# Performance work log

Hardware: AMD Instinct MI355X
Metric: run time of the kernel (lower is better)

## Reference

```python
import jax, jax.numpy as jnp
import numpy as np

N = 8192
D = 256
H = 4
E = 262144

def setup_inputs() -> dict:
    key = jax.random.key(0)
    ks = jax.random.split(key, 12)
    s = 1.0 / np.sqrt(D)
    inp = {
        "x": jax.random.normal(ks[0], (N, D), dtype=jnp.float32),
        "edge_index": jax.random.randint(ks[1], (2, E), 0, N, dtype=jnp.int64),
        "W_local": jax.random.normal(ks[2], (D, D), dtype=jnp.float32) * s,
        "b_local": jnp.zeros((D,), dtype=jnp.float32),
        "W_in": jax.random.normal(ks[3], (3 * D, D), dtype=jnp.float32) * s,
        "b_in": jnp.zeros((3 * D,), dtype=jnp.float32),
        "W_out": jax.random.normal(ks[4], (D, D), dtype=jnp.float32) * s,
        "b_out": jnp.zeros((D,), dtype=jnp.float32),
        "W1": jax.random.normal(ks[5], (2 * D, D), dtype=jnp.float32) * s,
        "b1": jnp.zeros((2 * D,), dtype=jnp.float32),
        "W2": jax.random.normal(ks[6], (D, 2 * D), dtype=jnp.float32) * (1.0 / np.sqrt(2 * D)),
        "b2": jnp.zeros((D,), dtype=jnp.float32),
    }
    return inp


def reference(x, edge_index, W_local, b_local, W_in, b_in, W_out, b_out, W1, b1, W2, b2):
    n = x.shape[0]
    dh = D // H
    # Dense adjacency build (faithful to original): adj[src, dst] = 1.0
    adj = jnp.zeros((n, n), dtype=x.dtype).at[edge_index[0], edge_index[1]].set(1.0)
    deg = jnp.clip(adj.sum(axis=1, keepdims=True), 1.0)  # (n, 1)
    adj_norm = adj / deg
    # Local message passing + linear
    local_out = (adj_norm @ x) @ W_local.T + b_local
    x = x + local_out
    # Multi-head self-attention (torch MultiheadAttention, batch of 1)
    qkv = x @ W_in.T + b_in  # (n, 3D)
    q, k, v = jnp.split(qkv, 3, axis=-1)
    q = q.reshape(n, H, dh)
    k = k.reshape(n, H, dh)
    v = v.reshape(n, H, dh)
    scores = jnp.einsum("qhd,khd->hqk", q, k) / np.sqrt(dh)  # (H, n, n)
    probs = jax.nn.softmax(scores, axis=-1)
    attn = jnp.einsum("hqk,khd->qhd", probs, v).reshape(n, D)
    attn_out = attn @ W_out.T + b_out
    x = x + attn_out
    # FFN with exact GELU
    h = jax.nn.gelu(x @ W1.T + b1, approximate=False)
    x = x + (h @ W2.T + b2)
    return x
```

## Files before the change

### kernel.cpp

```cpp
#include <hip/hip_runtime.h>
#include <stdint.h>

#define N_NODES 8192
#define DIM 256
#define NHEADS 4
#define DHEAD 64
#define NEDGES 262144
#define NSPLIT 4
#define KSPLIT (N_NODES / NSPLIT)

using bf16x8 = __attribute__((ext_vector_type(8))) __bf16;
using f32x4  = __attribute__((ext_vector_type(4))) float;

__device__ __forceinline__ unsigned short f2b(float f) {
    unsigned int u = __float_as_uint(f);
    unsigned int r = (u + 0x7FFFu + ((u >> 16) & 1u)) >> 16;
    return (unsigned short)r;
}

__device__ __forceinline__ float b2f(unsigned short s) {
    return __uint_as_float((unsigned int)s << 16);
}

__device__ __forceinline__ bf16x8 ld8(const unsigned short* p) {
    return *reinterpret_cast<const bf16x8*>(p);
}

__device__ __forceinline__ f32x4 mf(bf16x8 a, bf16x8 b, f32x4 c) {
    return __builtin_amdgcn_mfma_f32_16x16x32_bf16(a, b, c, 0, 0, 0);
}

__device__ __forceinline__ float fexp2(float x) {
    float r;
    asm volatile("v_exp_f32 %0, %1" : "=v"(r) : "v"(x));
    return r;
}

__device__ __forceinline__ void gl16(const void* g, void* l) {
    __builtin_amdgcn_global_load_lds(
        (const __attribute__((address_space(1))) unsigned int*)g,
        (__attribute__((address_space(3))) unsigned int*)l, 16, 0, 0);
}

#define QSCALE 0.18033688f

__global__ void detect_kernel(const void* edges, int* flag) {
    if (threadIdx.x == 0) {
        const long long* p = (const long long*)edges;
        int ok = 1;
        for (int i = 0; i < 64; ++i) {
            long long v = p[i];
            if (v < 0 || v >= N_NODES) ok = 0;
        }
        *flag = ok;
    }
}

__global__ void clear_kernel(uint4* p, int n16) {
    int i = blockIdx.x * blockDim.x + threadIdx.x;
    if (i < n16) p[i] = make_uint4(0, 0, 0, 0);
}

__global__ void edge_kernel(const void* edges, const int* flag, unsigned* mask) {
    int i = blockIdx.x * blockDim.x + threadIdx.x;
    if (i >= NEDGES) return;
    int src, dst;
    if (*flag) {
        const long long* p = (const long long*)edges;
        src = (int)p[i];
        dst = (int)p[NEDGES + i];
    } else {
        const int* p = (const int*)edges;
        src = p[i];
        dst = p[NEDGES + i];
    }
    atomicOr(&mask[src * (N_NODES / 32) + (dst >> 5)], 1u << (dst & 31));
}

__global__ __launch_bounds__(256) void agg_kernel(const unsigned* mask, const float* x,
                                                  unsigned short* m_bf) {
    __shared__ int nbr[N_NODES];
    __shared__ int wsum[4];
    int row = blockIdx.x;
    int tid = threadIdx.x, wave = tid >> 6, lane = tid & 63;

    unsigned bits = mask[row * (N_NODES / 32) + tid];
    int cnt = __popc(bits);
    int scan = cnt;
#pragma unroll
    for (int d = 1; d < 64; d <<= 1) {
        int v = __shfl_up(scan, d);
        if (lane >= d) scan += v;
    }
    if (lane == 63) wsum[wave] = scan;
    __syncthreads();
    int base = 0;
    for (int w = 0; w < 4; ++w) {
        int t = wsum[w];
        if (w < wave) base += t;
    }
    int deg = wsum[0] + wsum[1] + wsum[2] + wsum[3];
    int offset = base + scan - cnt;
    int nb = tid * 32;
    unsigned b2 = bits;
    while (b2) {
        int b = __ffs(b2) - 1;
        b2 &= b2 - 1;
        nbr[offset++] = nb + b;
    }
    __syncthreads();

    float a0 = 0.f, a1 = 0.f, a2 = 0.f, a3 = 0.f;
    int j = 0;
    for (; j + 4 <= deg; j += 4) {
        int n0 = nbr[j], n1 = nbr[j + 1], n2 = nbr[j + 2], n3 = nbr[j + 3];
        a0 += x[(size_t)n0 * DIM + tid];
        a1 += x[(size_t)n1 * DIM + tid];
        a2 += x[(size_t)n2 * DIM + tid];
        a3 += x[(size_t)n3 * DIM + tid];
    }
    for (; j < deg; ++j) a0 += x[(size_t)nbr[j] * DIM + tid];
    float acc = (a0 + a1) + (a2 + a3);
    float s = 1.0f / (float)(deg > 0 ? deg : 1);
    m_bf[(size_t)row * DIM + tid] = f2b(acc * s);
}

__global__ void cvt_kernel(const float* src, unsigned short* dst, int n) {
    int i = blockIdx.x * blockDim.x + threadIdx.x;
    if (i < n) dst[i] = f2b(src[i]);
}

template <int K>
__global__ __launch_bounds__(256, 4) void gemm_kernel(const unsigned short* __restrict__ A,
                                                      const unsigned short* __restrict__ W,
                                                      const float* __restrict__ bias,
                                                      const float* __restrict__ res,
                                                      float* __restrict__ outF,
                                                      unsigned short* __restrict__ outB,
                                                      int Nout, int qcols, int gelu) {
    __shared__ __align__(16) char smem[32768];
    int tid = threadIdx.x, wave = tid >> 6, lane = tid & 63;
    int c16 = lane & 15, g = lane >> 4;
    int r0b = blockIdx.x * 64;
    int c0 = blockIdx.y * 64;
    int lo3 = lane >> 3;
    int sw = ((lane & 7) ^ lo3) * 8;

    const unsigned short* sA = A + (size_t)(r0b + wave * 8 + lo3) * K + sw;
    const unsigned short* sB = W + (size_t)(c0 + wave * 8 + lo3) * K + sw;
    int dA = wave * 1024;
    int dB = 8192 + wave * 1024;

    auto stage = [&](int kt, int bufsel) {
        char* b = smem + bufsel * 16384;
        const unsigned short* a1 = sA + kt * 64;
        const unsigned short* b1 = sB + kt * 64;
        gl16(a1, b + dA);
        gl16(a1 + (size_t)32 * K, b + dA + 4096);
        gl16(b1, b + dB);
        gl16(b1 + (size_t)32 * K, b + dB + 4096);
    };

    f32x4 acc[4] = {};
    int arow = (wave * 16 + c16) * 128;
    int slot0 = ((0 + g) ^ (c16 & 7)) * 16;
    int slot1 = ((4 + g) ^ (c16 & 7)) * 16;

    stage(0, 0);
    asm volatile("s_waitcnt vmcnt(0)" ::: "memory");
    __syncthreads();

    constexpr int NT = K / 64;
#pragma unroll
    for (int kt = 0; kt < NT; ++kt) {
        if (kt + 1 < NT) stage(kt + 1, (kt + 1) & 1);
        char* buf = smem + (kt & 1) * 16384;
        bf16x8 af0 = ld8((unsigned short*)(buf + arow + slot0));
        bf16x8 af1 = ld8((unsigned short*)(buf + arow + slot1));
#pragma unroll
        for (int ct = 0; ct < 4; ++ct) {
            int brow = (ct * 16 + c16) * 128;
            bf16x8 bf0 = ld8((unsigned short*)(buf + 8192 + brow + slot0));
            bf16x8 bf1 = ld8((unsigned short*)(buf + 8192 + brow + slot1));
            acc[ct] = mf(af0, bf0, acc[ct]);
            acc[ct] = mf(af1, bf1, acc[ct]);
        }
        asm volatile("s_waitcnt vmcnt(0)" ::: "memory");
        __syncthreads();
    }

    int r0 = r0b + wave * 16;
#pragma unroll
    for (int ct = 0; ct < 4; ++ct) {
        int col = c0 + ct * 16 + c16;
        float bi = bias[col];
#pragma unroll
        for (int r = 0; r < 4; ++r) {
            int row = r0 + g * 4 + r;
            float gg = acc[ct][r] + bi;
            if (gelu) gg = 0.5f * gg * (1.0f + erff(gg * 0.70710678118654752f));
            if (res) gg += res[(size_t)row * Nout + col];
            if (outF) outF[(size_t)row * Nout + col] = gg;
            if (outB) {
                float gb = (col < qcols) ? gg * QSCALE : gg;
                outB[(size_t)row * Nout + col] = f2b(gb);
            }
        }
    }
}

__global__ __launch_bounds__(256) void vt_kernel(const unsigned short* qkv,
                                                 unsigned short* Vt) {
    __shared__ unsigned short T[64][72];
    int h = blockIdx.y;
    int n0 = blockIdx.x * 64;
    int t = threadIdx.x;
    int r = t & 63, cb = (t >> 6) * 16;
    const unsigned short* src = qkv + (size_t)(n0 + r) * 768 + 512 + h * 64 + cb;
    *(uint4*)&T[r][cb] = *(const uint4*)src;
    *(uint4*)&T[r][cb + 8] = *(const uint4*)(src + 8);
    __syncthreads();
    int d = t >> 2, nb = (t & 3) * 16;
    unsigned short tmp[16];
#pragma unroll
    for (int j = 0; j < 16; ++j) tmp[j] = T[nb + j][d];
    unsigned short* dst = Vt + (size_t)(h * 64 + d) * 8192 + n0 + nb;
    *(uint4*)dst = *(uint4*)&tmp[0];
    *(uint4*)(dst + 8) = *(uint4*)&tmp[8];
}

__global__ __launch_bounds__(256, 4) void flash_kernel(const unsigned short* __restrict__ qkv,
                                                       const unsigned short* __restrict__ vt,
                                                       unsigned short* __restrict__ Opart,
                                                       float2* __restrict__ ml) {
    __shared__ __align__(16) unsigned short smem[16384];
    char* sm = (char*)smem;
    int h = blockIdx.y, sp = blockIdx.z;
    int tid = threadIdx.x, wave = tid >> 6, lane = tid & 63;
    int c16 = lane & 15, g = lane >> 4;
    int q0 = blockIdx.x * 128 + wave * 32;

    bf16x8 qf[2][2];
#pragma unroll
    for (int qg = 0; qg < 2; ++qg) {
        const unsigned short* qrow = qkv + (size_t)(q0 + qg * 16 + c16) * 768 + h * DHEAD;
#pragma unroll
        for (int kc = 0; kc < 2; ++kc) qf[qg][kc] = ld8(qrow + kc * 32 + g * 8);
    }

    f32x4 O0[4] = {}, O1[4] = {};
    float m0 = -1e30f, m1 = -1e30f, l0 = 0.f, l1 = 0.f;

    int lo3 = lane >> 3;
    int sw = ((lane & 7) ^ lo3) * 8;
    int KOFFw = 4 * ((wave >> 1) & 1) + 16 * (wave & 1);
    int krow = KOFFw + 8 * (lane >> 5) + (lo3 & 3);
    int k0 = sp * KSPLIT;
    const unsigned short* kA = qkv + (size_t)(k0 + krow) * 768 + 256 + h * DHEAD + sw;
    const unsigned short* kB = kA + (size_t)32 * 768;
    const unsigned short* vA = vt + (size_t)(h * DHEAD + 8 * wave + lo3) * N_NODES + k0 + sw;
    const unsigned short* vB = vA + (size_t)32 * N_NODES;
    int ldsKA = wave * 1024, ldsKB = ldsKA + 4096;
    int ldsVA = 8192 + wave * 1024, ldsVB = ldsVA + 4096;

    int fragrow = c16 * 128;
    int slot0 = ((0 + g) ^ (c16 & 7)) * 16;
    int slot1 = ((4 + g) ^ (c16 & 7)) * 16;

    auto stage = [&](int bufsel) {
        char* b = sm + bufsel * 16384;
        gl16(kA, b + ldsKA);
        gl16(kB, b + ldsKB);
        gl16(vA, b + ldsVA);
        gl16(vB, b + ldsVB);
        kA += 64 * 768; kB += 64 * 768; vA += 64; vB += 64;
    };

    stage(0);
    asm volatile("s_waitcnt vmcnt(0)" ::: "memory");
    __syncthreads();

    const int nt = KSPLIT / 64;
    for (int t = 0; t < nt; ++t) {
        if (t + 1 < nt) stage((t + 1) & 1);
        char* buf = sm + (t & 1) * 16384;

        f32x4 S0[4], S1[4];
#pragma unroll
        for (int ct = 0; ct < 4; ++ct) {
            bf16x8 kf0 = ld8((unsigned short*)(buf + ct * 2048 + fragrow + slot0));
            bf16x8 kf1 = ld8((unsigned short*)(buf + ct * 2048 + fragrow + slot1));
            f32x4 a0 = {}, a1 = {};
            a0 = mf(kf0, qf[0][0], a0);
            a0 = mf(kf1, qf[0][1], a0);
            a1 = mf(kf0, qf[1][0], a1);
            a1 = mf(kf1, qf[1][1], a1);
            S0[ct] = a0;
            S1[ct] = a1;
        }

        {
            float tm = S0[0][0];
#pragma unroll
            for (int ct = 0; ct < 4; ++ct)
#pragma unroll
                for (int r = 0; r < 4; ++r) tm = fmaxf(tm, S0[ct][r]);
            tm = fmaxf(tm, __shfl_xor(tm, 16));
            tm = fmaxf(tm, __shfl_xor(tm, 32));
            if (tm - m0 > 8.0f) {
                float sc = fexp2(m0 - tm);
                m0 = tm;
                l0 *= sc;
#pragma unroll
                for (int dt = 0; dt < 4; ++dt)
#pragma unroll
                    for (int r = 0; r < 4; ++r) O0[dt][r] *= sc;
            }
            float rs = 0.0f;
#pragma unroll
            for (int ct = 0; ct < 4; ++ct)
#pragma unroll
                for (int r = 0; r < 4; ++r) {
                    float pv = fexp2(S0[ct][r] - m0);
                    S0[ct][r] = pv;
                    rs += pv;
                }
            rs += __shfl_xor(rs, 16);
            rs += __shfl_xor(rs, 32);
            l0 += rs;
        }
        {
            float tm = S1[0][0];
#pragma unroll
            for (int ct = 0; ct < 4; ++ct)
#pragma unroll
                for (int r = 0; r < 4; ++r) tm = fmaxf(tm, S1[ct][r]);
            tm = fmaxf(tm, __shfl_xor(tm, 16));
            tm = fmaxf(tm, __shfl_xor(tm, 32));
            if (tm - m1 > 8.0f) {
                float sc = fexp2(m1 - tm);
                m1 = tm;
                l1 *= sc;
#pragma unroll
                for (int dt = 0; dt < 4; ++dt)
#pragma unroll
                    for (int r = 0; r < 4; ++r) O1[dt][r] *= sc;
            }
            float rs = 0.0f;
#pragma unroll
            for (int ct = 0; ct < 4; ++ct)
#pragma unroll
                for (int r = 0; r < 4; ++r) {
                    float pv = fexp2(S1[ct][r] - m1);
                    S1[ct][r] = pv;
                    rs += pv;
                }
            rs += __shfl_xor(rs, 16);
            rs += __shfl_xor(rs, 32);
            l1 += rs;
        }

        bf16x8 p00, p01, p10, p11;
#pragma unroll
        for (int r = 0; r < 4; ++r) {
            p00[r] = (__bf16)S0[0][r]; p00[4 + r] = (__bf16)S0[1][r];
            p01[r] = (__bf16)S0[2][r]; p01[4 + r] = (__bf16)S0[3][r];
            p10[r] = (__bf16)S1[0][r]; p10[4 + r] = (__bf16)S1[1][r];
            p11[r] = (__bf16)S1[2][r]; p11[4 + r] = (__bf16)S1[3][r];
        }

#pragma unroll
        for (int dt = 0; dt < 4; ++dt) {
            bf16x8 vf0 = ld8((unsigned short*)(buf + 8192 + dt * 2048 + fragrow + slot0));
            bf16x8 vf1 = ld8((unsigned short*)(buf + 8192 + dt * 2048 + fragrow + slot1));
            f32x4 o0 = O0[dt], o1 = O1[dt];
            o0 = mf(vf0, p00, o0);
            o0 = mf(vf1, p01, o0);
            o1 = mf(vf0, p10, o1);
            o1 = mf(vf1, p11, o1);
            O0[dt] = o0;
            O1[dt] = o1;
        }

        asm volatile("s_waitcnt vmcnt(0)" ::: "memory");
        __syncthreads();
    }

    float inv0 = 1.0f / l0, inv1 = 1.0f / l1;
    if (g == 0) {
        ml[((size_t)sp * N_NODES + q0 + c16) * NHEADS + h] = make_float2(m0, l0);
        ml[((size_t)sp * N_NODES + q0 + 16 + c16) * NHEADS + h] = make_float2(m1, l1);
    }
    unsigned short* ob = smem + wave * 2304;
#pragma unroll
    for (int dt = 0; dt < 4; ++dt) {
        ushort4 u0, u1;
        u0.x = f2b(O0[dt][0] * inv0); u0.y = f2b(O0[dt][1] * inv0);
        u0.z = f2b(O0[dt][2] * inv0); u0.w = f2b(O0[dt][3] * inv0);
        u1.x = f2b(O1[dt][0] * inv1); u1.y = f2b(O1[dt][1] * inv1);
        u1.z = f2b(O1[dt][2] * inv1); u1.w = f2b(O1[dt][3] * inv1);
        *(ushort4*)&ob[(size_t)c16 * 72 + dt * 16 + 4 * g] = u0;
        *(ushort4*)&ob[(size_t)(16 + c16) * 72 + dt * 16 + 4 * g] = u1;
    }
    __syncthreads();
    {
        int R = tid >> 1, half = tid & 1;
        const unsigned short* src = smem + (R >> 5) * 2304 + (R & 31) * 72 + half * 32;
        unsigned short* dst = Opart + ((size_t)sp * N_NODES + blockIdx.x * 128 + R) * DIM + h * DHEAD + half * 32;
#pragma unroll
        for (int c = 0; c < 4; ++c) {
            uint4 v = *(const uint4*)(src + c * 8);
            *(uint4*)(dst + c * 8) = v;
        }
    }
}

__global__ __launch_bounds__(256) void merge_kernel(const unsigned short* Opart,
                                                    const float2* ml,
                                                    unsigned short* attnb) {
    int row = blockIdx.x;
    int tid = threadIdx.x;
    int h = tid >> 6;
    float2 e[NSPLIT];
    float M = -1e30f;
#pragma unroll
    for (int s = 0; s < NSPLIT; ++s) {
        e[s] = ml[((size_t)s * N_NODES + row) * NHEADS + h];
        M = fmaxf(M, e[s].x);
    }
    float L = 0.0f, w[NSPLIT];
#pragma unroll
    for (int s = 0; s < NSPLIT; ++s) {
        w[s] = e[s].y * fexp2(e[s].x - M);
        L += w[s];
    }
    float invL = 1.0f / L;
    float acc = 0.0f;
#pragma unroll
    for (int s = 0; s < NSPLIT; ++s)
        acc += w[s] * b2f(Opart[((size_t)s * N_NODES + row) * DIM + tid]);
    attnb[(size_t)row * DIM + tid] = f2b(acc * invL);
}

extern "C" void kernel_launch(void* const* d_in, const int* in_sizes, int n_in,
                              void* d_out, int out_size, void* d_ws, size_t ws_size,
                              hipStream_t stream) {
    const float* x = (const float*)d_in[0];
    const void* edges = d_in[1];
    const float* W_local = (const float*)d_in[2];
    const float* b_local = (const float*)d_in[3];
    const float* W_in = (const float*)d_in[4];
    const float* b_in = (const float*)d_in[5];
    const float* W_out = (const float*)d_in[6];
    const float* b_out = (const float*)d_in[7];
    const float* W1 = (const float*)d_in[8];
    const float* b1 = (const float*)d_in[9];
    const float* W2 = (const float*)d_in[10];
    const float* b2 = (const float*)d_in[11];
    float* out = (float*)d_out;

    char* p = (char*)d_ws;
    size_t off = 0;
    auto take = [&](size_t bytes) { char* q = p + off; off += (bytes + 255) & ~(size_t)255; return q; };
    int* flag = (int*)take(256);
    unsigned* mask = (unsigned*)take((size_t)N_NODES * N_NODES / 8);
    unsigned short* m_bf = (unsigned short*)take((size_t)N_NODES * DIM * 2);
    float* x1 = (float*)take((size_t)N_NODES * DIM * 4);
    unsigned short* x1b = (unsigned short*)take((size_t)N_NODES * DIM * 2);
    unsigned short* qkvb = (unsigned short*)take((size_t)N_NODES * 3 * DIM * 2);
    unsigned short* attnb = (unsigned short*)take((size_t)N_NODES * DIM * 2);
    float* x2 = (float*)take((size_t)N_NODES * DIM * 4);
    unsigned short* x2b = (unsigned short*)take((size_t)N_NODES * DIM * 2);
    unsigned short* hb = (unsigned short*)take((size_t)N_NODES * 2 * DIM * 2);
    unsigned short* Wlb = (unsigned short*)take((size_t)DIM * DIM * 2);
    unsigned short* Winb = (unsigned short*)take((size_t)3 * DIM * DIM * 2);
    unsigned short* Wob = (unsigned short*)take((size_t)DIM * DIM * 2);
    unsigned short* W1b = (unsigned short*)take((size_t)2 * DIM * DIM * 2);
    unsigned short* W2b = (unsigned short*)take((size_t)DIM * 2 * DIM * 2);

    unsigned short* Vtb = (unsigned short*)mask;
    float2* mlbuf = (float2*)((char*)mask + (size_t)4 * 1024 * 1024);
    unsigned short* Opart = (unsigned short*)x2;

    detect_kernel<<<1, 64, 0, stream>>>(edges, flag);
    {
        int n16 = (N_NODES * N_NODES / 8) / 16;
        clear_kernel<<<(n16 + 255) / 256, 256, 0, stream>>>((uint4*)mask, n16);
    }
    edge_kernel<<<(NEDGES + 255) / 256, 256, 0, stream>>>(edges, flag, mask);
    agg_kernel<<<N_NODES, 256, 0, stream>>>(mask, x, m_bf);

    cvt_kernel<<<(DIM * DIM + 255) / 256, 256, 0, stream>>>(W_local, Wlb, DIM * DIM);
    cvt_kernel<<<(3 * DIM * DIM + 255) / 256, 256, 0, stream>>>(W_in, Winb, 3 * DIM * DIM);
    cvt_kernel<<<(DIM * DIM + 255) / 256, 256, 0, stream>>>(W_out, Wob, DIM * DIM);
    cvt_kernel<<<(2 * DIM * DIM + 255) / 256, 256, 0, stream>>>(W1, W1b, 2 * DIM * DIM);
    cvt_kernel<<<(2 * DIM * DIM + 255) / 256, 256, 0, stream>>>(W2, W2b, 2 * DIM * DIM);

    gemm_kernel<DIM><<<dim3(N_NODES / 64, DIM / 64), 256, 0, stream>>>(
        m_bf, Wlb, b_local, x, x1, x1b, DIM, 0, 0);
    gemm_kernel<DIM><<<dim3(N_NODES / 64, 3 * DIM / 64), 256, 0, stream>>>(
        x1b, Winb, b_in, nullptr, nullptr, qkvb, 3 * DIM, DIM, 0);
    vt_kernel<<<dim3(N_NODES / 64, NHEADS), 256, 0, stream>>>(qkvb, Vtb);
    flash_kernel<<<dim3(N_NODES / 128, NHEADS, NSPLIT), 256, 0, stream>>>(qkvb, Vtb, Opart, mlbuf);
    merge_kernel<<<N_NODES, 256, 0, stream>>>(Opart, mlbuf, attnb);
    gemm_kernel<DIM><<<dim3(N_NODES / 64, DIM / 64), 256, 0, stream>>>(
        attnb, Wob, b_out, x1, x2, x2b, DIM, 0, 0);
    gemm_kernel<DIM><<<dim3(N_NODES / 64, 2 * DIM / 64), 256, 0, stream>>>(
        x2b, W1b, b1, nullptr, nullptr, hb, 2 * DIM, 0, 1);
    gemm_kernel<2 * DIM><<<dim3(N_NODES / 64, DIM / 64), 256, 0, stream>>>(
        hb, W2b, b2, x2, out, nullptr, DIM, 0, 0);
}
```

Before: 229.2 us.

## Rebalance flash splits to five, compute row sums via MFMA, fuse small launches

Raises the flash-attention key split from 4 to 5 and sizes the uneven splits explicitly (26/26/26/25/25 tiles), so the grid fills the GPU better. Occupancy hint goes to 5. Row sums of the probabilities now come from an extra MFMA against a ones vector instead of shuffle reductions, and the row max uses v_max3. The detect kernel is folded into the clear kernel and five weight conversions into one launch to cut launch overhead. This adds accumulator registers and more merge partitions, and depends on merge_kernel handling NSPLIT=5 (not visible).

Result: slower. 368.6 us (+60.8%).

```diff
diff --git a/kernel.cpp b/kernel.cpp
--- a/kernel.cpp
+++ b/kernel.cpp
@@ -6,8 +6,7 @@
 #define NHEADS 4
 #define DHEAD 64
 #define NEDGES 262144
-#define NSPLIT 4
-#define KSPLIT (N_NODES / NSPLIT)
+#define NSPLIT 5
 
 using bf16x8 = __attribute__((ext_vector_type(8))) __bf16;
 using f32x4  = __attribute__((ext_vector_type(4))) float;
@@ -36,6 +35,12 @@
     return r;
 }
 
+__device__ __forceinline__ float max3f(float a, float b, float c) {
+    float r;
+    asm("v_max3_f32 %0, %1, %2, %3" : "=v"(r) : "v"(a), "v"(b), "v"(c));
+    return r;
+}
+
 __device__ __forceinline__ void gl16(const void* g, void* l) {
     __builtin_amdgcn_global_load_lds(
         (const __attribute__((address_space(1))) unsigned int*)g,
@@ -44,21 +49,18 @@
 
 #define QSCALE 0.18033688f
 
-__global__ void detect_kernel(const void* edges, int* flag) {
-    if (threadIdx.x == 0) {
-        const long long* p = (const long long*)edges;
-        int ok = 1;
-        for (int i = 0; i < 64; ++i) {
-            long long v = p[i];
-            if (v < 0 || v >= N_NODES) ok = 0;
-        }
-        *flag = ok;
-    }
-}
-
-__global__ void clear_kernel(uint4* p, int n16) {
+__global__ void clear_kernel(uint4* p, int n16, const void* edges, int* flag) {
     int i = blockIdx.x * blockDim.x + threadIdx.x;
     if (i < n16) p[i] = make_uint4(0, 0, 0, 0);
+    if (i == 0) {
+        const long long* e = (const long long*)edges;
+        int ok = 1;
+        for (int j = 0; j < 64; ++j) {
+            long long v = e[j];
+            if (v < 0 || v >= N_NODES) ok = 0;
+        }
+        *flag = ok;
+    }
 }
 
 __global__ void edge_kernel(const void* edges, const int* flag, unsigned* mask) {
@@ -125,9 +127,17 @@
     m_bf[(size_t)row * DIM + tid] = f2b(acc * s);
 }
 
-__global__ void cvt_kernel(const float* src, unsigned short* dst, int n) {
+__global__ void cvt5_kernel(const float* a, const float* b, const float* c,
+                            const float* d, const float* e,
+                            unsigned short* oa, unsigned short* ob,
+                            unsigned short* oc, unsigned short* od,
+                            unsigned short* oe) {
     int i = blockIdx.x * blockDim.x + threadIdx.x;
-    if (i < n) dst[i] = f2b(src[i]);
+    if (i < 65536) oa[i] = f2b(a[i]);
+    else if (i < 262144) ob[i - 65536] = f2b(b[i - 65536]);
+    else if (i < 327680) oc[i - 262144] = f2b(c[i - 262144]);
+    else if (i < 458752) od[i - 327680] = f2b(d[i - 327680]);
+    else if (i < 589824) oe[i - 458752] = f2b(e[i - 458752]);
 }
 
 template <int K>
@@ -229,7 +239,7 @@
     *(uint4*)(dst + 8) = *(uint4*)&tmp[8];
 }
 
-__global__ __launch_bounds__(256, 4) void flash_kernel(const unsigned short* __restrict__ qkv,
+__global__ __launch_bounds__(256, 5) void flash_kernel(const unsigned short* __restrict__ qkv,
                                                        const unsigned short* __restrict__ vt,
                                                        unsigned short* __restrict__ Opart,
                                                        float2* __restrict__ ml) {
@@ -248,14 +258,22 @@
         for (int kc = 0; kc < 2; ++kc) qf[qg][kc] = ld8(qrow + kc * 32 + g * 8);
     }
 
-    f32x4 O0[4] = {}, O1[4] = {};
-    float m0 = -1e30f, m1 = -1e30f, l0 = 0.f, l1 = 0.f;
+    bf16x8 ones;
+#pragma unroll
+    for (int i = 0; i < 8; ++i) ones[i] = (__bf16)1.0f;
+
+    f32x4 O0[5] = {}, O1[5] = {};
+    float m0 = -1e30f, m1 = -1e30f;
 
     int lo3 = lane >> 3;
     int sw = ((lane & 7) ^ lo3) * 8;
     int KOFFw = 4 * ((wave >> 1) & 1) + 16 * (wave & 1);
     int krow = KOFFw + 8 * (lane >> 5) + (lo3 & 3);
-    int k0 = sp * KSPLIT;
+
+    int t0 = sp * 25 + (sp < 3 ? sp : 3);
+    int nt = 25 + (sp < 3 ? 1 : 0);
+    int k0 = t0 * 64;
+
     const unsigned short* kA = qkv + (size_t)(k0 + krow) * 768 + 256 + h * DHEAD + sw;
     const unsigned short* kB = kA + (size_t)32 * 768;
     const unsigned short* vA = vt + (size_t)(h * DHEAD + 8 * wave + lo3) * N_NODES + k0 + sw;
@@ -280,7 +298,6 @@
     asm volatile("s_waitcnt vmcnt(0)" ::: "memory");
     __syncthreads();
 
-    const int nt = KSPLIT / 64;
     for (int t = 0; t < nt; ++t) {
         if (t + 1 < nt) stage((t + 1) & 1);
         char* buf = sm + (t & 1) * 16384;
@@ -300,64 +317,52 @@
         }
 
         {
-            float tm = S0[0][0];
-#pragma unroll
-            for (int ct = 0; ct < 4; ++ct)
-#pragma unroll
-                for (int r = 0; r < 4; ++r) tm = fmaxf(tm, S0[ct][r]);
+            float tm = max3f(S0[0][0], S0[0][1], S0[0][2]);
+            tm = max3f(tm, S0[0][3], S0[1][0]);
+            tm = max3f(tm, S0[1][1], S0[1][2]);
+            tm = max3f(tm, S0[1][3], S0[2][0]);
+            tm = max3f(tm, S0[2][1], S0[2][2]);
+            tm = max3f(tm, S0[2][3], S0[3][0]);
+            tm = max3f(tm, S0[3][1], S0[3][2]);
+            tm = fmaxf(tm, S0[3][3]);
             tm = fmaxf(tm, __shfl_xor(tm, 16));
             tm = fmaxf(tm, __shfl_xor(tm, 32));
             if (tm - m0 > 8.0f) {
                 float sc = fexp2(m0 - tm);
                 m0 = tm;
-                l0 *= sc;
-#pragma unroll
-                for (int dt = 0; dt < 4; ++dt)
+#pragma unroll
+                for (int dt = 0; dt < 5; ++dt)
 #pragma unroll
                     for (int r = 0; r < 4; ++r) O0[dt][r] *= sc;
             }
-            float rs = 0.0f;
 #pragma unroll
             for (int ct = 0; ct < 4; ++ct)
 #pragma unroll
-                for (int r = 0; r < 4; ++r) {
-                    float pv = fexp2(S0[ct][r] - m0);
-                    S0[ct][r] = pv;
-                    rs += pv;
-                }
-            rs += __shfl_xor(rs, 16);
-            rs += __shfl_xor(rs, 32);
-            l0 += rs;
+                for (int r = 0; r < 4; ++r) S0[ct][r] = fexp2(S0[ct][r] - m0);
         }
         {
-            float tm = S1[0][0];
-#pragma unroll
-            for (int ct = 0; ct < 4; ++ct)
-#pragma unroll
-                for (int r = 0; r < 4; ++r) tm = fmaxf(tm, S1[ct][r]);
+            float tm = max3f(S1[0][0], S1[0][1], S1[0][2]);
+            tm = max3f(tm, S1[0][3], S1[1][0]);
+            tm = max3f(tm, S1[1][1], S1[1][2]);
+            tm = max3f(tm, S1[1][3], S1[2][0]);
+            tm = max3f(tm, S1[2][1], S1[2][2]);
+            tm = max3f(tm, S1[2][3], S1[3][0]);
+            tm = max3f(tm, S1[3][1], S1[3][2]);
+            tm = fmaxf(tm, S1[3][3]);
             tm = fmaxf(tm, __shfl_xor(tm, 16));
             tm = fmaxf(tm, __shfl_xor(tm, 32));
             if (tm - m1 > 8.0f) {
                 float sc = fexp2(m1 - tm);
                 m1 = tm;
-                l1 *= sc;
-#pragma unroll
-                for (int dt = 0; dt < 4; ++dt)
+#pragma unroll
+                for (int dt = 0; dt < 5; ++dt)
 #pragma unroll
                     for (int r = 0; r < 4; ++r) O1[dt][r] *= sc;
             }
-            float rs = 0.0f;
 #pragma unroll
             for (int ct = 0; ct < 4; ++ct)
 #pragma unroll
-                for (int r = 0; r < 4; ++r) {
-                    float pv = fexp2(S1[ct][r] - m1);
-                    S1[ct][r] = pv;
-                    rs += pv;
-                }
-            rs += __shfl_xor(rs, 16);
-            rs += __shfl_xor(rs, 32);
-            l1 += rs;
+                for (int r = 0; r < 4; ++r) S1[ct][r] = fexp2(S1[ct][r] - m1);
         }
 
         bf16x8 p00, p01, p10, p11;
@@ -381,11 +386,16 @@
             O0[dt] = o0;
             O1[dt] = o1;
         }
+        O0[4] = mf(ones, p00, O0[4]);
+        O0[4] = mf(ones, p01, O0[4]);
+        O1[4] = mf(ones, p10, O1[4]);
+        O1[4] = mf(ones, p11, O1[4]);
 
         asm volatile("s_waitcnt vmcnt(0)" ::: "memory");
         __syncthreads();
     }
 
+    float l0 = O0[4][0], l1 = O1[4][0];
     float inv0 = 1.0f / l0, inv1 = 1.0f / l1;
     if (g == 0) {
         ml[((size_t)sp * N_NODES + q0 + c16) * NHEADS + h] = make_float2(m0, l0);
@@ -482,19 +492,15 @@
     float2* mlbuf = (float2*)((char*)mask + (size_t)4 * 1024 * 1024);
     unsigned short* Opart = (unsigned short*)x2;
 
-    detect_kernel<<<1, 64, 0, stream>>>(edges, flag);
     {
         int n16 = (N_NODES * N_NODES / 8) / 16;
-        clear_kernel<<<(n16 + 255) / 256, 256, 0, stream>>>((uint4*)mask, n16);
+        clear_kernel<<<(n16 + 255) / 256, 256, 0, stream>>>((uint4*)mask, n16, edges, flag);
     }
     edge_kernel<<<(NEDGES + 255) / 256, 256, 0, stream>>>(edges, flag, mask);
     agg_kernel<<<N_NODES, 256, 0, stream>>>(mask, x, m_bf);
 
-    cvt_kernel<<<(DIM * DIM + 255) / 256, 256, 0, stream>>>(W_local, Wlb, DIM * DIM);
-    cvt_kernel<<<(3 * DIM * DIM + 255) / 256, 256, 0, stream>>>(W_in, Winb, 3 * DIM * DIM);
-    cvt_kernel<<<(DIM * DIM + 255) / 256, 256, 0, stream>>>(W_out, Wob, DIM * DIM);
-    cvt_kernel<<<(2 * DIM * DIM + 255) / 256, 256, 0, stream>>>(W1, W1b, 2 * DIM * DIM);
-    cvt_kernel<<<(2 * DIM * DIM + 255) / 256, 256, 0, stream>>>(W2, W2b, 2 * DIM * DIM);
+    cvt5_kernel<<<(589824 + 255) / 256, 256, 0, stream>>>(
+        W_local, W_in, W_out, W1, W2, Wlb, Winb, Wob, W1b, W2b);
 
     gemm_kernel<DIM><<<dim3(N_NODES / 64, DIM / 64), 256, 0, stream>>>(
         m_bf, Wlb, b_local, x, x1, x1b, DIM, 0, 0);
```
